# Kernel tuning notes

Measured on AMD Instinct MI355X. Metric: run time of the kernel, lower is better.

The kernel has to match this reference:

```python
import jax, jax.numpy as jnp
import numpy as np

N, E = 50000, 800000
DIN, DH, DOUT = 128, 128, 64


def setup_inputs() -> dict:
    key = jax.random.key(0)
    ks = jax.random.split(key, 18)
    s = 0.05
    inp = {
        "x": jax.random.normal(ks[0], (N, DIN), dtype=jnp.float32),
        "edge_index": jax.random.randint(ks[1], (2, E), 0, N, dtype=jnp.int64),
        # conv1 MLP: Linear(DIN,DH), Linear(DH,DH)
        "c1_w1": jax.random.normal(ks[2], (DIN, DH), dtype=jnp.float32) * s,
        "c1_b1": jax.random.normal(ks[3], (DH,), dtype=jnp.float32) * s,
        "c1_w2": jax.random.normal(ks[4], (DH, DH), dtype=jnp.float32) * s,
        "c1_b2": jax.random.normal(ks[5], (DH,), dtype=jnp.float32) * s,
        # conv2 MLP
        "c2_w1": jax.random.normal(ks[6], (DH, DH), dtype=jnp.float32) * s,
        "c2_b1": jax.random.normal(ks[7], (DH,), dtype=jnp.float32) * s,
        "c2_w2": jax.random.normal(ks[8], (DH, DH), dtype=jnp.float32) * s,
        "c2_b2": jax.random.normal(ks[9], (DH,), dtype=jnp.float32) * s,
        # conv3 MLP
        "c3_w1": jax.random.normal(ks[10], (DH, DH), dtype=jnp.float32) * s,
        "c3_b1": jax.random.normal(ks[11], (DH,), dtype=jnp.float32) * s,
        "c3_w2": jax.random.normal(ks[12], (DH, DH), dtype=jnp.float32) * s,
        "c3_b2": jax.random.normal(ks[13], (DH,), dtype=jnp.float32) * s,
        # output head
        "lin1_w": jax.random.normal(ks[14], (DH, DH), dtype=jnp.float32) * s,
        "lin1_b": jax.random.normal(ks[15], (DH,), dtype=jnp.float32) * s,
        "lin2_w": jax.random.normal(ks[16], (DH, DOUT), dtype=jnp.float32) * s,
        "lin2_b": jax.random.normal(ks[17], (DOUT,), dtype=jnp.float32) * s,
    }
    return inp


def _gin_conv(h, src, dst, w1, b1, w2, b2):
    # PyG GINConv, eps=0: MLP((1+eps)*x + sum_{j->i} x_j)
    agg = jax.ops.segment_sum(h[src], dst, num_segments=h.shape[0])  # [N, D]
    z = h + agg
    z = jax.nn.relu(z @ w1 + b1)
    return jax.nn.relu(z @ w2 + b2)


def reference(x, edge_index, c1_w1, c1_b1, c1_w2, c1_b2,
              c2_w1, c2_b1, c2_w2, c2_b2,
              c3_w1, c3_b1, c3_w2, c3_b2,
              lin1_w, lin1_b, lin2_w, lin2_b):
    src, dst = edge_index[0], edge_index[1]
    h = _gin_conv(x, src, dst, c1_w1, c1_b1, c1_w2, c1_b2)
    h = jax.nn.relu(h)  # redundant after MLP ReLU, but faithful to source
    h = _gin_conv(h, src, dst, c2_w1, c2_b1, c2_w2, c2_b2)
    h = jax.nn.relu(h)
    h = _gin_conv(h, src, dst, c3_w1, c3_b1, c3_w2, c3_b2)
    h = jax.nn.relu(h @ lin1_w + lin1_b)
    return h @ lin2_w + lin2_b  # [N, DOUT]
```

## Files before the change

kernel.cpp:

```cpp
#include <hip/hip_runtime.h>
#include <hip/hip_bf16.h>

typedef __attribute__((ext_vector_type(8))) short bf16x8;
typedef __attribute__((ext_vector_type(4))) float f32x4;

#define DH 128
#define DOUT 64

static __device__ __forceinline__ unsigned short f2bf(float f) {
    __hip_bfloat16 h = __float2bfloat16(f);
    return *(unsigned short*)&h;
}
static __device__ __forceinline__ void acc2(float& a0, float& a1, unsigned int u) {
    a0 += __uint_as_float(u << 16);
    a1 += __uint_as_float(u & 0xffff0000u);
}


struct WPrep {
    const float* src[8];
    unsigned short* dst[8];
};

__global__ void prep_kernel(const float* __restrict__ x, unsigned short* __restrict__ xb,
                            unsigned short* __restrict__ hA, unsigned short* __restrict__ hB,
                            int n4, WPrep p,
                            int* __restrict__ cnt, int* __restrict__ rank,
                            const int* __restrict__ dstv, int E, int N_) {
    int id = blockIdx.x * blockDim.x + threadIdx.x;
    if (id < n4) {
        float4 v = ((const float4*)x)[id];
        ushort4 b;
        b.x = f2bf(v.x); b.y = f2bf(v.y); b.z = f2bf(v.z); b.w = f2bf(v.w);
        ((ushort4*)xb)[id] = b;
        return;
    }
    id -= n4;
    if (id < 7 * 16384 + 8192) {
        int m, off;
        if (id < 7 * 16384) { m = id >> 14; off = id & 16383; }
        else { m = 7; off = id - 7 * 16384; }
        int shift = (m == 7) ? 6 : 7;
        int nc = 1 << shift;
        int k = off >> shift;
        int n = off & (nc - 1);
        p.dst[m][n * 128 + k] = f2bf(p.src[m][off]);
        return;
    }
    id -= 7 * 16384 + 8192;
    if (id < 3 * 128) {
        int j = id & 127, w = id >> 7;
        if (w == 0) xb[(size_t)N_ * 128 + j] = 0;
        else if (w == 1) hA[(size_t)N_ * 128 + j] = 0;
        else hB[(size_t)N_ * 128 + j] = 0;
        return;
    }
    id -= 384;
    if (id < E) {
        int d = dstv[id];
        if ((unsigned)d < (unsigned)N_) rank[id] = atomicAdd(&cnt[d], 1);
    }
}


__global__ void scan1_kernel(const int* __restrict__ cnt, int* __restrict__ rp_part,
                             int* __restrict__ bsum, int n) {
    __shared__ int s[256];
    int tid = threadIdx.x;
    int i = blockIdx.x * 256 + tid;
    int v = (i < n) ? ((cnt[i] + 7) & ~7) : 0;
    s[tid] = v;
    __syncthreads();
    for (int off = 1; off < 256; off <<= 1) {
        int t = (tid >= off) ? s[tid - off] : 0;
        __syncthreads();
        s[tid] += t;
        __syncthreads();
    }
    if (i <= n) rp_part[i] = s[tid] - v;
    if (tid == 255) bsum[blockIdx.x] = s[255];
}

__global__ void scan2_kernel(int* __restrict__ bsum, int nb) {
    __shared__ int s[256];
    int tid = threadIdx.x;
    int v = (tid < nb) ? bsum[tid] : 0;
    s[tid] = v;
    __syncthreads();
    for (int off = 1; off < 256; off <<= 1) {
        int t = (tid >= off) ? s[tid - off] : 0;
        __syncthreads();
        s[tid] += t;
        __syncthreads();
    }
    if (tid < nb) bsum[tid] = s[tid] - v;
}

__global__ void scan3_fill_kernel(const int* __restrict__ rp_part, const int* __restrict__ bsum,
                                  int* __restrict__ row_ptr,
                                  const int* __restrict__ src, const int* __restrict__ dst,
                                  const int* __restrict__ rank, const int* __restrict__ cnt,
                                  int* __restrict__ esrc,
                                  int n, int E) {
    int gid = blockIdx.x * blockDim.x + threadIdx.x;
    if (gid <= n) row_ptr[gid] = rp_part[gid] + bsum[gid >> 8];
    if (gid < n) {
        int st = rp_part[gid] + bsum[gid >> 8];
        int c = cnt[gid];
        int pe = (c + 7) & ~7;
        int zr = n << 8;
        for (int j = c; j < pe; ++j) esrc[st + j] = zr;
    }
    if (gid < E) {
        int d = dst[gid];
        if ((unsigned)d < (unsigned)n)
            esrc[rp_part[d] + bsum[d >> 8] + rank[gid]] = src[gid] << 8;
    }
}


#define ACC8(i, U) \
    _Pragma("unroll") for (int z = 0; z < 8; ++z) acc2(a0[i], a1[i], U[z]);

#define LOAD8(U) \
    if (q < t) { \
        int _o = q - p0; \
        _Pragma("unroll") for (int z = 0; z < 8; ++z) { \
            unsigned _ix = (unsigned)sIdx[_o + z]; \
            U[z] = *(const unsigned*)(hc + _ix + voff); \
        } \
        q += 8; \
    }

#define STEP(U) \
    if (r < t) { \
        int nn = (r >= sE0 ? 1 : 0) + (r >= sE1 ? 1 : 0) + (r >= sE2 ? 1 : 0); \
        if (nn == 0) { ACC8(0, U) } \
        else if (nn == 1) { ACC8(1, U) } \
        else if (nn == 2) { ACC8(2, U) } \
        else { ACC8(3, U) } \
        r += 8; \
        LOAD8(U) \
    }

template <bool HEAD>
__launch_bounds__(256, 7)
__global__ void layer_kernel(const unsigned short* __restrict__ h,
                             const int* __restrict__ rp,
                             const int* __restrict__ esrc,
                             const unsigned short* __restrict__ W1t,
                             const float* __restrict__ b1,
                             const unsigned short* __restrict__ W2t,
                             const float* __restrict__ b2,
                             const unsigned short* __restrict__ W3t,
                             const float* __restrict__ b3,
                             const unsigned short* __restrict__ W4t,
                             const float* __restrict__ b4,
                             void* __restrict__ outp, int M) {
    constexpr int LDA = 128 + 8;
    constexpr int CAP = 2048;
    __shared__ __align__(16) unsigned short As[16][LDA];
    __shared__ __align__(16) unsigned short Zs[16][LDA];
    __shared__ int sIdx[CAP];

    int tid = threadIdx.x;
    int wave = __builtin_amdgcn_readfirstlane(tid >> 6);
    int lane = tid & 63;
    int row0 = blockIdx.x * 16;
    int nd0 = row0 + wave * 4;

    const char* hc = (const char*)h;
    unsigned voff = (unsigned)lane << 2;

    int wbv = rp[row0];
    int Cv = rp[min(row0 + 16, M)] - wbv;
    int wb = __builtin_amdgcn_readfirstlane(wbv);
    int C = __builtin_amdgcn_readfirstlane(Cv);

    int bv[5];
#pragma unroll
    for (int i = 0; i < 5; ++i) bv[i] = rp[min(nd0 + i, M)] - wb;
    int sB  = __builtin_amdgcn_readfirstlane(bv[0]);
    int sE0 = __builtin_amdgcn_readfirstlane(bv[1]);
    int sE1 = __builtin_amdgcn_readfirstlane(bv[2]);
    int sE2 = __builtin_amdgcn_readfirstlane(bv[3]);
    int sE3 = __builtin_amdgcn_readfirstlane(bv[4]);

    float a0[4] = {0.f, 0.f, 0.f, 0.f}, a1[4] = {0.f, 0.f, 0.f, 0.f};

    for (int p0 = 0; p0 < C; p0 += CAP) {
        int cend = min(C, p0 + CAP);
        for (int i = tid; i < cend - p0; i += 256) sIdx[i] = esrc[wb + p0 + i];
        __syncthreads();
        int s = max(sB, p0);
        int t = min(sE3, cend);
        if (s < t) {
            unsigned u0[8], u1[8], u2[8], u3[8];
            int q = s;
            LOAD8(u0) LOAD8(u1) LOAD8(u2) LOAD8(u3)
            int r = s;
            while (r < t) {
                STEP(u0) STEP(u1) STEP(u2) STEP(u3)
            }
        }
        __syncthreads();
    }

#pragma unroll
    for (int i = 0; i < 4; ++i) {
        int ndc = min(nd0 + i, M);
        unsigned su = *(const unsigned*)(hc + ((size_t)(unsigned)ndc << 8) + voff);
        acc2(a0[i], a1[i], su);
        unsigned pv = (unsigned)f2bf(a0[i]) | ((unsigned)f2bf(a1[i]) << 16);
        *(unsigned*)&As[wave * 4 + i][lane * 2] = pv;
    }
    __syncthreads();

    int quad = lane >> 4;
    int l16 = lane & 15;

    bf16x8 af[4];
#pragma unroll
    for (int kt = 0; kt < 4; ++kt)
        af[kt] = *(const bf16x8*)(&As[l16][kt * 32 + quad * 8]);
#pragma unroll
    for (int p = 0; p < 2; ++p) {
        int ncol = (wave * 2 + p) * 16 + l16;
        const unsigned short* wp = W1t + ncol * 128 + quad * 8;
        f32x4 a = {0.f, 0.f, 0.f, 0.f};
#pragma unroll
        for (int kt = 0; kt < 4; ++kt)
            a = __builtin_amdgcn_mfma_f32_16x16x32_bf16(
                af[kt], *(const bf16x8*)(wp + kt * 32), a, 0, 0, 0);
        float bs = b1[ncol];
#pragma unroll
        for (int r = 0; r < 4; ++r) {
            float v = a[r] + bs;
            if (v < 0.f) v = 0.f;
            Zs[quad * 4 + r][ncol] = f2bf(v);
        }
    }
    __syncthreads();

    bf16x8 zf[4];
#pragma unroll
    for (int kt = 0; kt < 4; ++kt)
        zf[kt] = *(const bf16x8*)(&Zs[l16][kt * 32 + quad * 8]);
#pragma unroll
    for (int p = 0; p < 2; ++p) {
        int ncol = (wave * 2 + p) * 16 + l16;
        const unsigned short* wp = W2t + ncol * 128 + quad * 8;
        f32x4 a = {0.f, 0.f, 0.f, 0.f};
#pragma unroll
        for (int kt = 0; kt < 4; ++kt)
            a = __builtin_amdgcn_mfma_f32_16x16x32_bf16(
                zf[kt], *(const bf16x8*)(wp + kt * 32), a, 0, 0, 0);
        float bs = b2[ncol];
#pragma unroll
        for (int r = 0; r < 4; ++r) {
            float v = a[r] + bs;
            if (v < 0.f) v = 0.f;
            if (HEAD) {
                As[quad * 4 + r][ncol] = f2bf(v);
            } else {
                int grow = row0 + quad * 4 + r;
                if (grow < M)
                    ((unsigned short*)outp)[(size_t)grow * 128 + ncol] = f2bf(v);
            }
        }
    }

    if (HEAD) {
        __syncthreads();
        bf16x8 hf[4];
#pragma unroll
        for (int kt = 0; kt < 4; ++kt)
            hf[kt] = *(const bf16x8*)(&As[l16][kt * 32 + quad * 8]);
#pragma unroll
        for (int p = 0; p < 2; ++p) {
            int ncol = (wave * 2 + p) * 16 + l16;
            const unsigned short* wp = W3t + ncol * 128 + quad * 8;
            f32x4 a = {0.f, 0.f, 0.f, 0.f};
#pragma unroll
            for (int kt = 0; kt < 4; ++kt)
                a = __builtin_amdgcn_mfma_f32_16x16x32_bf16(
                    hf[kt], *(const bf16x8*)(wp + kt * 32), a, 0, 0, 0);
            float bs = b3[ncol];
#pragma unroll
            for (int r = 0; r < 4; ++r) {
                float v = a[r] + bs;
                if (v < 0.f) v = 0.f;
                Zs[quad * 4 + r][ncol] = f2bf(v);
            }
        }
        __syncthreads();
        bf16x8 gf[4];
#pragma unroll
        for (int kt = 0; kt < 4; ++kt)
            gf[kt] = *(const bf16x8*)(&Zs[l16][kt * 32 + quad * 8]);
        {
            int ncol = wave * 16 + l16;
            const unsigned short* wp = W4t + ncol * 128 + quad * 8;
            f32x4 a = {0.f, 0.f, 0.f, 0.f};
#pragma unroll
            for (int kt = 0; kt < 4; ++kt)
                a = __builtin_amdgcn_mfma_f32_16x16x32_bf16(
                    gf[kt], *(const bf16x8*)(wp + kt * 32), a, 0, 0, 0);
            float bs = b4[ncol];
#pragma unroll
            for (int r = 0; r < 4; ++r) {
                int grow = row0 + quad * 4 + r;
                if (grow < M)
                    ((float*)outp)[(size_t)grow * 64 + ncol] = a[r] + bs;
            }
        }
    }
}


extern "C" void kernel_launch(void* const* d_in, const int* in_sizes, int n_in,
                              void* d_out, int out_size, void* d_ws, size_t ws_size,
                              hipStream_t stream) {
    const float* x = (const float*)d_in[0];
    const int* ei = (const int*)d_in[1];
    int N = in_sizes[0] / DH;
    int E = in_sizes[1] / 2;
    const int* src = ei;
    const int* dstv = ei + E;
    int Epad = E + 7 * N + 1024;

    char* ws = (char*)d_ws;
    size_t off = 0;
    auto alloc = [&](size_t bytes) -> void* {
        void* p = ws + off;
        off += (bytes + 255) & ~(size_t)255;
        return p;
    };
    unsigned short* xb = (unsigned short*)alloc((size_t)(N + 1) * DH * 2);
    unsigned short* hA = (unsigned short*)alloc((size_t)(N + 1) * DH * 2);
    unsigned short* hB = (unsigned short*)alloc((size_t)(N + 1) * DH * 2);
    unsigned short* wt[8];
    for (int m = 0; m < 8; ++m) wt[m] = (unsigned short*)alloc(16384 * 2);
    int* cnt     = (int*)alloc((size_t)N * 4);
    int* rp_part = (int*)alloc((size_t)(N + 1) * 4);
    int* row_ptr = (int*)alloc((size_t)(N + 1) * 4);
    int* rank    = (int*)alloc((size_t)E * 4);
    int* bsum    = (int*)alloc(256 * 4);
    int* esrc    = (int*)alloc((size_t)Epad * 4);

    WPrep wp;
    wp.src[0] = (const float*)d_in[2];
    wp.src[1] = (const float*)d_in[4];
    wp.src[2] = (const float*)d_in[6];
    wp.src[3] = (const float*)d_in[8];
    wp.src[4] = (const float*)d_in[10];
    wp.src[5] = (const float*)d_in[12];
    wp.src[6] = (const float*)d_in[14];
    wp.src[7] = (const float*)d_in[16];
    for (int m = 0; m < 8; ++m) wp.dst[m] = wt[m];

    hipMemsetAsync(cnt, 0, (size_t)N * 4, stream);

    int n4 = N * DH / 4;
    int prep_items = n4 + 7 * 16384 + 8192 + 384 + E;
    prep_kernel<<<(prep_items + 255) / 256, 256, 0, stream>>>(
        x, xb, hA, hB, n4, wp, cnt, rank, dstv, E, N);

    int nb = (N + 1 + 255) / 256;
    int eb = (E + 255) / 256;
    scan1_kernel<<<nb, 256, 0, stream>>>(cnt, rp_part, bsum, N);
    scan2_kernel<<<1, 256, 0, stream>>>(bsum, nb);
    scan3_fill_kernel<<<eb, 256, 0, stream>>>(rp_part, bsum, row_ptr,
                                              src, dstv, rank, cnt, esrc, N, E);

    int gb = (N + 15) / 16;

    const float* c1b1 = (const float*)d_in[3];
    const float* c1b2 = (const float*)d_in[5];
    const float* c2b1 = (const float*)d_in[7];
    const float* c2b2 = (const float*)d_in[9];
    const float* c3b1 = (const float*)d_in[11];
    const float* c3b2 = (const float*)d_in[13];
    const float* l1b  = (const float*)d_in[15];
    const float* l2b  = (const float*)d_in[17];

    layer_kernel<false><<<gb, 256, 0, stream>>>(
        xb, row_ptr, esrc, wt[0], c1b1, wt[1], c1b2,
        nullptr, nullptr, nullptr, nullptr, hA, N);
    layer_kernel<false><<<gb, 256, 0, stream>>>(
        hA, row_ptr, esrc, wt[2], c2b1, wt[3], c2b2,
        nullptr, nullptr, nullptr, nullptr, hB, N);
    layer_kernel<true><<<gb, 256, 0, stream>>>(
        hB, row_ptr, esrc, wt[4], c3b1, wt[5], c3b2,
        wt[6], l1b, wt[7], l2b, d_out, N);
}
```

Baseline: 323.1 us.

## Partition CSR edges by source-node chunk to improve gather locality

Builds the CSR as NC separate partitions keyed by source-node chunk (src >> 14), so each destination row's neighbours are grouped by source range. The layer kernel walks the chunks in order, which is meant to keep the gathered source rows within a smaller window that fits better in L2/MALL. The cost is about four times as many rows to count, scan and pad: the per-row padding to a multiple of 8 now applies to every (chunk, row) pair, adding padding edges. The gather loop also gains extra row_ptr reads and block barriers per chunk, and scan2 is widened to 1024 threads.

```diff
diff --git a/kernel.cpp b/kernel.cpp
--- a/kernel.cpp
+++ b/kernel.cpp
@@ -6,6 +6,7 @@
 
 #define DH 128
 #define DOUT 64
+#define CSH 14
 
 static __device__ __forceinline__ unsigned short f2bf(float f) {
     __hip_bfloat16 h = __float2bfloat16(f);
@@ -26,7 +27,8 @@
                             unsigned short* __restrict__ hA, unsigned short* __restrict__ hB,
                             int n4, WPrep p,
                             int* __restrict__ cnt, int* __restrict__ rank,
-                            const int* __restrict__ dstv, int E, int N_) {
+                            const int* __restrict__ srcv, const int* __restrict__ dstv,
+                            int E, int N_, int csh) {
     int id = blockIdx.x * blockDim.x + threadIdx.x;
     if (id < n4) {
         float4 v = ((const float4*)x)[id];
@@ -58,7 +60,10 @@
     id -= 384;
     if (id < E) {
         int d = dstv[id];
-        if ((unsigned)d < (unsigned)N_) rank[id] = atomicAdd(&cnt[d], 1);
+        if ((unsigned)d < (unsigned)N_) {
+            int c = (unsigned)srcv[id] >> csh;
+            rank[id] = atomicAdd(&cnt[c * N_ + d], 1);
+        }
     }
 }
 
@@ -82,12 +87,12 @@
 }
 
 __global__ void scan2_kernel(int* __restrict__ bsum, int nb) {
-    __shared__ int s[256];
+    __shared__ int s[1024];
     int tid = threadIdx.x;
     int v = (tid < nb) ? bsum[tid] : 0;
     s[tid] = v;
     __syncthreads();
-    for (int off = 1; off < 256; off <<= 1) {
+    for (int off = 1; off < 1024; off <<= 1) {
         int t = (tid >= off) ? s[tid - off] : 0;
         __syncthreads();
         s[tid] += t;
@@ -101,10 +106,10 @@
                                   const int* __restrict__ src, const int* __restrict__ dst,
                                   const int* __restrict__ rank, const int* __restrict__ cnt,
                                   int* __restrict__ esrc,
-                                  int n, int E) {
+                                  int n, int nrows, int E, int csh) {
     int gid = blockIdx.x * blockDim.x + threadIdx.x;
-    if (gid <= n) row_ptr[gid] = rp_part[gid] + bsum[gid >> 8];
-    if (gid < n) {
+    if (gid <= nrows) row_ptr[gid] = rp_part[gid] + bsum[gid >> 8];
+    if (gid < nrows) {
         int st = rp_part[gid] + bsum[gid >> 8];
         int c = cnt[gid];
         int pe = (c + 7) & ~7;
@@ -113,8 +118,11 @@
     }
     if (gid < E) {
         int d = dst[gid];
-        if ((unsigned)d < (unsigned)n)
-            esrc[rp_part[d] + bsum[d >> 8] + rank[gid]] = src[gid] << 8;
+        if ((unsigned)d < (unsigned)n) {
+            int ch = (unsigned)src[gid] >> csh;
+            int row = ch * n + d;
+            esrc[rp_part[row] + bsum[row >> 8] + rank[gid]] = src[gid] << 8;
+        }
     }
 }
 
@@ -156,7 +164,7 @@
                              const float* __restrict__ b3,
                              const unsigned short* __restrict__ W4t,
                              const float* __restrict__ b4,
-                             void* __restrict__ outp, int M) {
+                             void* __restrict__ outp, int M, int NC) {
     constexpr int LDA = 128 + 8;
     constexpr int CAP = 2048;
     __shared__ __align__(16) unsigned short As[16][LDA];
@@ -172,38 +180,42 @@
     const char* hc = (const char*)h;
     unsigned voff = (unsigned)lane << 2;
 
-    int wbv = rp[row0];
-    int Cv = rp[min(row0 + 16, M)] - wbv;
-    int wb = __builtin_amdgcn_readfirstlane(wbv);
-    int C = __builtin_amdgcn_readfirstlane(Cv);
-
-    int bv[5];
-#pragma unroll
-    for (int i = 0; i < 5; ++i) bv[i] = rp[min(nd0 + i, M)] - wb;
-    int sB  = __builtin_amdgcn_readfirstlane(bv[0]);
-    int sE0 = __builtin_amdgcn_readfirstlane(bv[1]);
-    int sE1 = __builtin_amdgcn_readfirstlane(bv[2]);
-    int sE2 = __builtin_amdgcn_readfirstlane(bv[3]);
-    int sE3 = __builtin_amdgcn_readfirstlane(bv[4]);
-
     float a0[4] = {0.f, 0.f, 0.f, 0.f}, a1[4] = {0.f, 0.f, 0.f, 0.f};
 
-    for (int p0 = 0; p0 < C; p0 += CAP) {
-        int cend = min(C, p0 + CAP);
-        for (int i = tid; i < cend - p0; i += 256) sIdx[i] = esrc[wb + p0 + i];
-        __syncthreads();
-        int s = max(sB, p0);
-        int t = min(sE3, cend);
-        if (s < t) {
-            unsigned u0[8], u1[8], u2[8], u3[8];
-            int q = s;
-            LOAD8(u0) LOAD8(u1) LOAD8(u2) LOAD8(u3)
-            int r = s;
-            while (r < t) {
-                STEP(u0) STEP(u1) STEP(u2) STEP(u3)
+    for (int c = 0; c < NC; ++c) {
+        int base = c * M;
+        int wbv = rp[base + row0];
+        int Cv = rp[base + min(row0 + 16, M)] - wbv;
+        int wb = __builtin_amdgcn_readfirstlane(wbv);
+        int C = __builtin_amdgcn_readfirstlane(Cv);
+        if (C == 0) continue;
+
+        int bv[5];
+#pragma unroll
+        for (int i = 0; i < 5; ++i) bv[i] = rp[base + min(nd0 + i, M)] - wb;
+        int sB  = __builtin_amdgcn_readfirstlane(bv[0]);
+        int sE0 = __builtin_amdgcn_readfirstlane(bv[1]);
+        int sE1 = __builtin_amdgcn_readfirstlane(bv[2]);
+        int sE2 = __builtin_amdgcn_readfirstlane(bv[3]);
+        int sE3 = __builtin_amdgcn_readfirstlane(bv[4]);
+
+        for (int p0 = 0; p0 < C; p0 += CAP) {
+            int cend = min(C, p0 + CAP);
+            for (int i = tid; i < cend - p0; i += 256) sIdx[i] = esrc[wb + p0 + i];
+            __syncthreads();
+            int s = max(sB, p0);
+            int t = min(sE3, cend);
+            if (s < t) {
+                unsigned u0[8], u1[8], u2[8], u3[8];
+                int q = s;
+                LOAD8(u0) LOAD8(u1) LOAD8(u2) LOAD8(u3)
+                int r = s;
+                while (r < t) {
+                    STEP(u0) STEP(u1) STEP(u2) STEP(u3)
+                }
             }
-        }
-        __syncthreads();
+            __syncthreads();
+        }
     }
 
 #pragma unroll
@@ -327,7 +339,29 @@
     int E = in_sizes[1] / 2;
     const int* src = ei;
     const int* dstv = ei + E;
-    int Epad = E + 7 * N + 1024;
+
+    auto calc = [&](int NCq) -> size_t {
+        size_t nrowsq = (size_t)NCq * N;
+        size_t Epadq = (size_t)E + 7 * nrowsq + 1024;
+        auto al = [](size_t b) { return (b + 255) & ~(size_t)255; };
+        size_t s = 0;
+        s += 3 * al((size_t)(N + 1) * DH * 2);
+        s += 8 * al(16384 * 2);
+        s += al(nrowsq * 4);
+        s += 2 * al((nrowsq + 1) * 4);
+        s += al((size_t)E * 4);
+        s += al(1024 * 4);
+        s += al(Epadq * 4);
+        return s;
+    };
+    int csh = CSH;
+    int NC = (N + (1 << csh) - 1) >> csh;
+    while (NC > 1 && calc(NC) > ws_size) {
+        csh++;
+        NC = (N + (1 << csh) - 1) >> csh;
+    }
+    int nrows = NC * N;
+    int Epad = E + nrows * 7 + 1024;
 
     char* ws = (char*)d_ws;
     size_t off = 0;
@@ -341,11 +375,11 @@
     unsigned short* hB = (unsigned short*)alloc((size_t)(N + 1) * DH * 2);
     unsigned short* wt[8];
     for (int m = 0; m < 8; ++m) wt[m] = (unsigned short*)alloc(16384 * 2);
-    int* cnt     = (int*)alloc((size_t)N * 4);
-    int* rp_part = (int*)alloc((size_t)(N + 1) * 4);
-    int* row_ptr = (int*)alloc((size_t)(N + 1) * 4);
+    int* cnt     = (int*)alloc((size_t)nrows * 4);
+    int* rp_part = (int*)alloc((size_t)(nrows + 1) * 4);
+    int* row_ptr = (int*)alloc((size_t)(nrows + 1) * 4);
     int* rank    = (int*)alloc((size_t)E * 4);
-    int* bsum    = (int*)alloc(256 * 4);
+    int* bsum    = (int*)alloc(1024 * 4);
     int* esrc    = (int*)alloc((size_t)Epad * 4);
 
     WPrep wp;
@@ -359,19 +393,19 @@
     wp.src[7] = (const float*)d_in[16];
     for (int m = 0; m < 8; ++m) wp.dst[m] = wt[m];
 
-    hipMemsetAsync(cnt, 0, (size_t)N * 4, stream);
+    hipMemsetAsync(cnt, 0, (size_t)nrows * 4, stream);
 
     int n4 = N * DH / 4;
     int prep_items = n4 + 7 * 16384 + 8192 + 384 + E;
     prep_kernel<<<(prep_items + 255) / 256, 256, 0, stream>>>(
-        x, xb, hA, hB, n4, wp, cnt, rank, dstv, E, N);
-
-    int nb = (N + 1 + 255) / 256;
-    int eb = (E + 255) / 256;
-    scan1_kernel<<<nb, 256, 0, stream>>>(cnt, rp_part, bsum, N);
-    scan2_kernel<<<1, 256, 0, stream>>>(bsum, nb);
-    scan3_fill_kernel<<<eb, 256, 0, stream>>>(rp_part, bsum, row_ptr,
-                                              src, dstv, rank, cnt, esrc, N, E);
+        x, xb, hA, hB, n4, wp, cnt, rank, src, dstv, E, N, csh);
+
+    int nb = (nrows + 1 + 255) / 256;
+    int fb = (max(nrows + 1, E) + 255) / 256;
+    scan1_kernel<<<nb, 256, 0, stream>>>(cnt, rp_part, bsum, nrows);
+    scan2_kernel<<<1, 1024, 0, stream>>>(bsum, nb);
+    scan3_fill_kernel<<<fb, 256, 0, stream>>>(rp_part, bsum, row_ptr,
+                                              src, dstv, rank, cnt, esrc, N, nrows, E, csh);
 
     int gb = (N + 15) / 16;
 
@@ -386,11 +420,11 @@
 
     layer_kernel<false><<<gb, 256, 0, stream>>>(
         xb, row_ptr, esrc, wt[0], c1b1, wt[1], c1b2,
-        nullptr, nullptr, nullptr, nullptr, hA, N);
+        nullptr, nullptr, nullptr, nullptr, hA, N, NC);
     layer_kernel<false><<<gb, 256, 0, stream>>>(
         hA, row_ptr, esrc, wt[2], c2b1, wt[3], c2b2,
-        nullptr, nullptr, nullptr, nullptr, hB, N);
+        nullptr, nullptr, nullptr, nullptr, hB, N, NC);
     layer_kernel<true><<<gb, 256, 0, stream>>>(
         hB, row_ptr, esrc, wt[4], c3b1, wt[5], c3b2,
-        wt[6], l1b, wt[7], l2b, d_out, N);
-}
+        wt[6], l1b, wt[7], l2b, d_out, N, NC);
+}
```

Result: slower. 332.1 us (+2.8%).

## Gather neighbor rows with 16-byte loads split across lane groups, then reduce

Applied to the files above, without the earlier changes.

Before, each lane loaded 4 bytes (one bf16 pair) per edge, so a wave read one 256-byte row per neighbor. Now each group of 16 lanes loads a whole row with uint4 loads and the four groups handle different edges (2 per group per step). Each lane keeps 8 partial sums per node, reduced across groups with xor shuffles before the self term is added and the result packed into LDS. This means fewer, wider gather instructions at the cost of more registers (accumulators go from 8 to 32), so the occupancy hint drops from 7 to 6.

```diff
diff --git a/kernel.cpp b/kernel.cpp
--- a/kernel.cpp
+++ b/kernel.cpp
@@ -119,16 +119,20 @@
 }
 
 
-#define ACC8(i, U) \
-    _Pragma("unroll") for (int z = 0; z < 8; ++z) acc2(a0[i], a1[i], U[z]);
+struct RP { uint4 a, b; };
+
+#define ACC8(i, U) { \
+    acc2(ac[i][0], ac[i][1], U.a.x); acc2(ac[i][2], ac[i][3], U.a.y); \
+    acc2(ac[i][4], ac[i][5], U.a.z); acc2(ac[i][6], ac[i][7], U.a.w); \
+    acc2(ac[i][0], ac[i][1], U.b.x); acc2(ac[i][2], ac[i][3], U.b.y); \
+    acc2(ac[i][4], ac[i][5], U.b.z); acc2(ac[i][6], ac[i][7], U.b.w); }
 
 #define LOAD8(U) \
     if (q < t) { \
         int _o = q - p0; \
-        _Pragma("unroll") for (int z = 0; z < 8; ++z) { \
-            unsigned _ix = (unsigned)sIdx[_o + z]; \
-            U[z] = *(const unsigned*)(hc + _ix + voff); \
-        } \
+        int2 _ip = *(const int2*)&sIdx[_o + 2 * lgrp]; \
+        U.a = *(const uint4*)(hc + (unsigned)_ip.x + voff16); \
+        U.b = *(const uint4*)(hc + (unsigned)_ip.y + voff16); \
         q += 8; \
     }
 
@@ -144,7 +148,7 @@
     }
 
 template <bool HEAD>
-__launch_bounds__(256, 7)
+__launch_bounds__(256, 6)
 __global__ void layer_kernel(const unsigned short* __restrict__ h,
                              const int* __restrict__ rp,
                              const int* __restrict__ esrc,
@@ -166,11 +170,12 @@
     int tid = threadIdx.x;
     int wave = __builtin_amdgcn_readfirstlane(tid >> 6);
     int lane = tid & 63;
+    int lgrp = lane >> 4;
     int row0 = blockIdx.x * 16;
     int nd0 = row0 + wave * 4;
 
     const char* hc = (const char*)h;
-    unsigned voff = (unsigned)lane << 2;
+    unsigned voff16 = (unsigned)(lane & 15) << 4;
 
     int wbv = rp[row0];
     int Cv = rp[min(row0 + 16, M)] - wbv;
@@ -186,7 +191,11 @@
     int sE2 = __builtin_amdgcn_readfirstlane(bv[3]);
     int sE3 = __builtin_amdgcn_readfirstlane(bv[4]);
 
-    float a0[4] = {0.f, 0.f, 0.f, 0.f}, a1[4] = {0.f, 0.f, 0.f, 0.f};
+    float ac[4][8];
+#pragma unroll
+    for (int i = 0; i < 4; ++i)
+#pragma unroll
+        for (int c = 0; c < 8; ++c) ac[i][c] = 0.f;
 
     for (int p0 = 0; p0 < C; p0 += CAP) {
         int cend = min(C, p0 + CAP);
@@ -195,7 +204,7 @@
         int s = max(sB, p0);
         int t = min(sE3, cend);
         if (s < t) {
-            unsigned u0[8], u1[8], u2[8], u3[8];
+            RP u0, u1, u2, u3;
             int q = s;
             LOAD8(u0) LOAD8(u1) LOAD8(u2) LOAD8(u3)
             int r = s;
@@ -207,12 +216,31 @@
     }
 
 #pragma unroll
-    for (int i = 0; i < 4; ++i) {
-        int ndc = min(nd0 + i, M);
-        unsigned su = *(const unsigned*)(hc + ((size_t)(unsigned)ndc << 8) + voff);
-        acc2(a0[i], a1[i], su);
-        unsigned pv = (unsigned)f2bf(a0[i]) | ((unsigned)f2bf(a1[i]) << 16);
-        *(unsigned*)&As[wave * 4 + i][lane * 2] = pv;
+    for (int i = 0; i < 4; ++i)
+#pragma unroll
+        for (int c = 0; c < 8; ++c) {
+            float v = ac[i][c];
+            v += __shfl_xor(v, 16);
+            v += __shfl_xor(v, 32);
+            ac[i][c] = v;
+        }
+
+    if (lane < 16) {
+#pragma unroll
+        for (int i = 0; i < 4; ++i) {
+            int ndc = min(nd0 + i, M);
+            uint4 sv = *(const uint4*)(hc + ((unsigned)ndc << 8) + voff16);
+            acc2(ac[i][0], ac[i][1], sv.x);
+            acc2(ac[i][2], ac[i][3], sv.y);
+            acc2(ac[i][4], ac[i][5], sv.z);
+            acc2(ac[i][6], ac[i][7], sv.w);
+            uint4 pk;
+            pk.x = (unsigned)f2bf(ac[i][0]) | ((unsigned)f2bf(ac[i][1]) << 16);
+            pk.y = (unsigned)f2bf(ac[i][2]) | ((unsigned)f2bf(ac[i][3]) << 16);
+            pk.z = (unsigned)f2bf(ac[i][4]) | ((unsigned)f2bf(ac[i][5]) << 16);
+            pk.w = (unsigned)f2bf(ac[i][6]) | ((unsigned)f2bf(ac[i][7]) << 16);
+            *(uint4*)&As[wave * 4 + i][lane * 8] = pk;
+        }
     }
     __syncthreads();
 
```

Measured after the change: 736.2 us. +127.9%, slower.

## Gather neighbors per 16-lane group with 16-byte loads and pad rows to two

Applied to the files above, without the earlier changes.

Each wave previously walked the four destination rows' edges one after another, with all 64 lanes loading 4 bytes per neighbor. Now each 16-lane group owns one destination row and loads 16 bytes per lane per neighbor, two neighbors at a time, with eight accumulators. CSR row padding drops from multiples of 8 to multiples of 2, so fewer dummy zero-row gathers are made. The cost is possible load imbalance across groups, since every group runs the loop count of the wave's longest row, and a lower occupancy bound (6 instead of 7).

```diff
diff --git a/kernel.cpp b/kernel.cpp
--- a/kernel.cpp
+++ b/kernel.cpp
@@ -68,7 +68,7 @@
     __shared__ int s[256];
     int tid = threadIdx.x;
     int i = blockIdx.x * 256 + tid;
-    int v = (i < n) ? ((cnt[i] + 7) & ~7) : 0;
+    int v = (i < n) ? ((cnt[i] + 1) & ~1) : 0;
     s[tid] = v;
     __syncthreads();
     for (int off = 1; off < 256; off <<= 1) {
@@ -107,7 +107,7 @@
     if (gid < n) {
         int st = rp_part[gid] + bsum[gid >> 8];
         int c = cnt[gid];
-        int pe = (c + 7) & ~7;
+        int pe = (c + 1) & ~1;
         int zr = n << 8;
         for (int j = c; j < pe; ++j) esrc[st + j] = zr;
     }
@@ -119,32 +119,30 @@
 }
 
 
-#define ACC8(i, U) \
-    _Pragma("unroll") for (int z = 0; z < 8; ++z) acc2(a0[i], a1[i], U[z]);
-
-#define LOAD8(U) \
-    if (q < t) { \
+struct RP { uint4 a, b; };
+
+#define ACC8(U) { \
+    acc2(ac[0], ac[1], U.a.x); acc2(ac[2], ac[3], U.a.y); \
+    acc2(ac[4], ac[5], U.a.z); acc2(ac[6], ac[7], U.a.w); \
+    acc2(ac[0], ac[1], U.b.x); acc2(ac[2], ac[3], U.b.y); \
+    acc2(ac[4], ac[5], U.b.z); acc2(ac[6], ac[7], U.b.w); }
+
+#define LOADP(U) \
+    if (q < ge) { \
         int _o = q - p0; \
-        _Pragma("unroll") for (int z = 0; z < 8; ++z) { \
-            unsigned _ix = (unsigned)sIdx[_o + z]; \
-            U[z] = *(const unsigned*)(hc + _ix + voff); \
-        } \
-        q += 8; \
-    }
-
-#define STEP(U) \
-    if (r < t) { \
-        int nn = (r >= sE0 ? 1 : 0) + (r >= sE1 ? 1 : 0) + (r >= sE2 ? 1 : 0); \
-        if (nn == 0) { ACC8(0, U) } \
-        else if (nn == 1) { ACC8(1, U) } \
-        else if (nn == 2) { ACC8(2, U) } \
-        else { ACC8(3, U) } \
-        r += 8; \
-        LOAD8(U) \
-    }
+        int2 _ip = *(const int2*)&sIdx[_o]; \
+        U.a = *(const uint4*)(hc + (unsigned)_ip.x + voff16); \
+        U.b = *(const uint4*)(hc + (unsigned)_ip.y + voff16); \
+        q += 2; \
+    }
+
+#define CONS(U) \
+    { if (r < ge) { ACC8(U) } \
+      r += 2; \
+      LOADP(U) }
 
 template <bool HEAD>
-__launch_bounds__(256, 7)
+__launch_bounds__(256, 6)
 __global__ void layer_kernel(const unsigned short* __restrict__ h,
                              const int* __restrict__ rp,
                              const int* __restrict__ esrc,
@@ -161,63 +159,71 @@
     constexpr int CAP = 2048;
     __shared__ __align__(16) unsigned short As[16][LDA];
     __shared__ __align__(16) unsigned short Zs[16][LDA];
-    __shared__ int sIdx[CAP];
+    __shared__ __align__(16) int sIdx[CAP];
 
     int tid = threadIdx.x;
     int wave = __builtin_amdgcn_readfirstlane(tid >> 6);
     int lane = tid & 63;
+    int lgrp = lane >> 4;
+    int l16 = lane & 15;
     int row0 = blockIdx.x * 16;
     int nd0 = row0 + wave * 4;
+    int nd = nd0 + lgrp;
 
     const char* hc = (const char*)h;
-    unsigned voff = (unsigned)lane << 2;
+    unsigned voff16 = (unsigned)l16 << 4;
 
     int wbv = rp[row0];
     int Cv = rp[min(row0 + 16, M)] - wbv;
     int wb = __builtin_amdgcn_readfirstlane(wbv);
     int C = __builtin_amdgcn_readfirstlane(Cv);
 
-    int bv[5];
-#pragma unroll
-    for (int i = 0; i < 5; ++i) bv[i] = rp[min(nd0 + i, M)] - wb;
-    int sB  = __builtin_amdgcn_readfirstlane(bv[0]);
-    int sE0 = __builtin_amdgcn_readfirstlane(bv[1]);
-    int sE1 = __builtin_amdgcn_readfirstlane(bv[2]);
-    int sE2 = __builtin_amdgcn_readfirstlane(bv[3]);
-    int sE3 = __builtin_amdgcn_readfirstlane(bv[4]);
-
-    float a0[4] = {0.f, 0.f, 0.f, 0.f}, a1[4] = {0.f, 0.f, 0.f, 0.f};
+    int bg = rp[min(nd, M)] - wb;
+    int eg = rp[min(nd + 1, M)] - wb;
+
+    float ac[8];
+#pragma unroll
+    for (int c = 0; c < 8; ++c) ac[c] = 0.f;
 
     for (int p0 = 0; p0 < C; p0 += CAP) {
         int cend = min(C, p0 + CAP);
         for (int i = tid; i < cend - p0; i += 256) sIdx[i] = esrc[wb + p0 + i];
         __syncthreads();
-        int s = max(sB, p0);
-        int t = min(sE3, cend);
-        if (s < t) {
-            unsigned u0[8], u1[8], u2[8], u3[8];
-            int q = s;
-            LOAD8(u0) LOAD8(u1) LOAD8(u2) LOAD8(u3)
-            int r = s;
-            while (r < t) {
-                STEP(u0) STEP(u1) STEP(u2) STEP(u3)
+        int gb = max(bg, p0);
+        int ge = min(eg, cend);
+        int v = ge - gb; if (v < 0) v = 0;
+        int mx = max(v, __shfl_xor(v, 16));
+        mx = max(mx, __shfl_xor(mx, 32));
+        int nloop = (__builtin_amdgcn_readfirstlane(mx) + 3) >> 2;
+        if (nloop) {
+            RP u0, u1;
+            int q = gb, r = gb;
+            LOADP(u0) LOADP(u1)
+            for (int it = 0; it < nloop; ++it) {
+                CONS(u0)
+                CONS(u1)
             }
         }
         __syncthreads();
     }
 
-#pragma unroll
-    for (int i = 0; i < 4; ++i) {
-        int ndc = min(nd0 + i, M);
-        unsigned su = *(const unsigned*)(hc + ((size_t)(unsigned)ndc << 8) + voff);
-        acc2(a0[i], a1[i], su);
-        unsigned pv = (unsigned)f2bf(a0[i]) | ((unsigned)f2bf(a1[i]) << 16);
-        *(unsigned*)&As[wave * 4 + i][lane * 2] = pv;
+    {
+        int ndc = min(nd, M);
+        uint4 sv = *(const uint4*)(hc + ((unsigned)ndc << 8) + voff16);
+        acc2(ac[0], ac[1], sv.x);
+        acc2(ac[2], ac[3], sv.y);
+        acc2(ac[4], ac[5], sv.z);
+        acc2(ac[6], ac[7], sv.w);
+        uint4 pk;
+        pk.x = (unsigned)f2bf(ac[0]) | ((unsigned)f2bf(ac[1]) << 16);
+        pk.y = (unsigned)f2bf(ac[2]) | ((unsigned)f2bf(ac[3]) << 16);
+        pk.z = (unsigned)f2bf(ac[4]) | ((unsigned)f2bf(ac[5]) << 16);
+        pk.w = (unsigned)f2bf(ac[6]) | ((unsigned)f2bf(ac[7]) << 16);
+        *(uint4*)&As[wave * 4 + lgrp][l16 * 8] = pk;
     }
     __syncthreads();
 
     int quad = lane >> 4;
-    int l16 = lane & 15;
 
     bf16x8 af[4];
 #pragma unroll
@@ -327,7 +333,7 @@
     int E = in_sizes[1] / 2;
     const int* src = ei;
     const int* dstv = ei + E;
-    int Epad = E + 7 * N + 1024;
+    int Epad = E + N + 1024;
 
     char* ws = (char*)d_ws;
     size_t off = 0;
```

New measurement: 331.0 us. +2.4%, slower.
